# Kernel optimization log

Hardware: AMD Instinct MI355X
Metric: run time of the kernel (lower is better)

The kernel has to match this reference:

```python
import jax, jax.numpy as jnp
import numpy as np

CODEBOOK_SIZE = 8192
EMBED_DIM = 256


def setup_inputs() -> dict:
    key = jax.random.key(0)
    k_rep, k_cb = jax.random.split(key)
    rep = jax.random.normal(k_rep, (32, 2048, EMBED_DIM), dtype=jnp.float32)
    codebook = jax.random.normal(k_cb, (CODEBOOK_SIZE, EMBED_DIM), dtype=jnp.float32)
    return {"rep": rep, "codebook": codebook}


def reference(rep, codebook):
    # rep: [B, M, D], codebook: [K, D]
    B, M, D = rep.shape
    rep_flat = rep.reshape(-1, D)                                # [B*M, D]
    a2 = jnp.sum(rep_flat * rep_flat, axis=1, keepdims=True)     # [B*M, 1]
    b2 = jnp.sum(codebook * codebook, axis=1)[None, :]           # [1, K]
    ab = rep_flat @ codebook.T                                   # [B*M, K]
    dist = a2 + b2 - 2.0 * ab                                    # [B*M, K]
    idx = jnp.argmin(dist, axis=1).reshape(B, M)                 # [B, M] int
    return idx
```

## Files before the change

### kernel.cpp

```cpp
#include <hip/hip_runtime.h>
#include <stdint.h>

#define KCODES 8192
#define DIM 256
#define BM 128
#define BN 128
#define NTHREADS 512
#define NKT (KCODES / BN)
#define NSTEP (NKT * 2)

typedef _Float16 h16;
typedef __attribute__((ext_vector_type(8))) _Float16 f16x8;
typedef __attribute__((ext_vector_type(4))) float f32x4;

__device__ __forceinline__ void split8(const float* __restrict__ x, f16x8& h, f16x8& l) {
    #pragma unroll
    for (int i = 0; i < 8; ++i) {
        float v = x[i];
        _Float16 hv = (_Float16)v;
        h[i] = hv;
        l[i] = (_Float16)(v - (float)hv);
    }
}

__device__ __forceinline__ unsigned int ford(float f) {
    unsigned int b = __float_as_uint(f);
    return (b & 0x80000000u) ? ~b : (b | 0x80000000u);
}

#define WS_C2H   0u
#define WS_LC    32768u
#define WS_CN    65536u
#define WS_CNT   98304u
#define WS_LIST  98560u
#define WS_CAND  360704u
#define WS_THR   622848u
#define WS_KEYS  917504u
#define WS_BPH   2097152u

__global__ __launch_bounds__(256) void c2x_kernel(const float* __restrict__ cb,
                                                  float* __restrict__ c2h,
                                                  float* __restrict__ lc,
                                                  float* __restrict__ cn, int K) {
    int w = (blockIdx.x * blockDim.x + threadIdx.x) >> 6;
    int lane = threadIdx.x & 63;
    if (w >= K) return;
    const float4 v = *(const float4*)(cb + (size_t)w * DIM + lane * 4);
    float s = 0.f, sr = 0.f;
    const float xs[4] = {v.x, v.y, v.z, v.w};
    #pragma unroll
    for (int i = 0; i < 4; ++i) {
        float x = xs[i];
        s += x * x;
        float hf = (float)(_Float16)x;
        float rho = x - hf;
        sr += rho * rho;
    }
    #pragma unroll
    for (int off = 32; off > 0; off >>= 1) { s += __shfl_down(s, off); sr += __shfl_down(sr, off); }
    if (lane == 0) { c2h[w] = 0.5f * s; cn[w] = sqrtf(s); lc[w] = sqrtf(sr); }
}

__global__ __launch_bounds__(256) void pack_h_kernel(const float* __restrict__ cb,
                                                     h16* __restrict__ Bp) {
    const int tid = blockIdx.x * 256 + threadIdx.x;
    const int code = tid >> 5;
    const int grp = tid & 31;
    float x[8];
    *(float4*)&x[0] = *(const float4*)(cb + (size_t)code * DIM + grp * 8);
    *(float4*)&x[4] = *(const float4*)(cb + (size_t)code * DIM + grp * 8 + 4);
    f16x8 hh;
    #pragma unroll
    for (int i = 0; i < 8; ++i) hh[i] = (_Float16)x[i];
    const int kt = code >> 7, col = code & 127;
    const int chunk = grp >> 2, g = grp & 3;
    const int P = kt * 4 + (chunk >> 1);
    const int s = (chunk & 1) * 4 + g;
    const int phys = s ^ (col & 7);
    *(f16x8*)(Bp + (size_t)P * 8192 + col * 64 + phys * 8) = hh;
}

__global__ __launch_bounds__(NTHREADS, 2) void vq_pass1(
    const float* __restrict__ rep, const h16* __restrict__ Bp,
    const float* __restrict__ c2h, const float* __restrict__ lcA,
    const float* __restrict__ cnA, int* __restrict__ cand,
    float* __restrict__ thr) {

    __shared__ __align__(16) h16 dbuf[2][16384];

    const int t = threadIdx.x;
    const int lane = t & 63;
    const int c15 = lane & 15;
    const int g = lane >> 4;
    const int w = t >> 6;
    const int wrow = (w >> 1) * 32;
    const int wcol = (w & 1) * 64;
    const int row0 = blockIdx.x * BM;

    f16x8 ah[2][8];
    float hn[2], rn[2];
    #pragma unroll
    for (int m = 0; m < 2; ++m) {
        const float* ar = rep + (size_t)(row0 + wrow + m * 16 + c15) * DIM + g * 8;
        float hs = 0.f, rs = 0.f;
        #pragma unroll
        for (int ch = 0; ch < 8; ++ch) {
            float x[8];
            *(float4*)&x[0] = *(const float4*)(ar + ch * 32);
            *(float4*)&x[4] = *(const float4*)(ar + ch * 32 + 4);
            #pragma unroll
            for (int i = 0; i < 8; ++i) {
                _Float16 hv = (_Float16)x[i];
                ah[m][ch][i] = hv;
                float hf = (float)hv;
                hs += hf * hf;
                float rho = x[i] - hf;
                rs += rho * rho;
            }
        }
        hs += __shfl_xor(hs, 16); hs += __shfl_xor(hs, 32);
        rs += __shfl_xor(rs, 16); rs += __shfl_xor(rs, 32);
        hn[m] = sqrtf(hs); rn[m] = sqrtf(rs);
    }

    f32x4 acc[2][4];
    float u1v[2][4], u2v[2][4], B2[2][4];
    int u1i[2][4];
    #pragma unroll
    for (int m = 0; m < 2; ++m)
        #pragma unroll
        for (int n = 0; n < 4; ++n) {
            #pragma unroll
            for (int r = 0; r < 4; ++r) acc[m][n][r] = 0.f;
            u1v[m][n] = -3.4e38f; u2v[m][n] = -3.4e38f; u1i[m][n] = 0;
        }

    auto issueStep = [&](int s2, int b) {
        const h16* src = Bp + (size_t)s2 * 16384 + t * 8;
        h16* dst = &dbuf[b][t * 8];
        #pragma unroll
        for (int i = 0; i < 4; ++i)
            __builtin_amdgcn_global_load_lds(
                (const __attribute__((address_space(1))) uint32_t*)(src + i * 4096),
                (__attribute__((address_space(3))) uint32_t*)(dst + i * 4096),
                16, 0, 0);
    };

    asm volatile("s_waitcnt vmcnt(0)" ::: "memory");
    issueStep(0, 0);

    #pragma unroll 1
    for (int kt = 0; kt < NKT; ++kt) {
        const int ktbase = kt * BN;
        #pragma unroll
        for (int q = 0; q < 2; ++q) {
            const int s = kt * 2 + q;
            asm volatile("s_waitcnt vmcnt(0) lgkmcnt(0)" ::: "memory");
            __builtin_amdgcn_s_barrier();
            __builtin_amdgcn_sched_barrier(0);

            if (q == 0) {
                #pragma unroll
                for (int n = 0; n < 4; ++n) {
                    const int col = ktbase + wcol + n * 16 + c15;
                    float cc = c2h[col], lv = lcA[col], cv = cnA[col];
                    #pragma unroll
                    for (int m = 0; m < 2; ++m)
                        B2[m][n] = hn[m] * lv + rn[m] * cv + 0.012f - cc;
                }
            }
            if (s + 1 < NSTEP) issueStep(s + 1, q ^ 1);

            const h16* lb = &dbuf[q][0];
            #pragma unroll
            for (int j = 0; j < 4; ++j) {
                const int ch = q * 4 + j;
                const h16* lp = lb + (j >> 1) * 8192;
                #pragma unroll
                for (int n = 0; n < 4; ++n) {
                    const int base = (wcol + n * 16 + c15) * 64;
                    f16x8 bh = *(const f16x8*)&lp[base + ((((j & 1) * 4 + g) ^ (c15 & 7)) << 3)];
                    #pragma unroll
                    for (int m = 0; m < 2; ++m)
                        acc[m][n] = __builtin_amdgcn_mfma_f32_16x16x32_f16(ah[m][ch], bh, acc[m][n], 0, 0, 0);
                }
            }

            if (q == 1) {
                #pragma unroll
                for (int n = 0; n < 4; ++n) {
                    const int col = ktbase + wcol + n * 16 + c15;
                    #pragma unroll
                    for (int m = 0; m < 2; ++m)
                        #pragma unroll
                        for (int r = 0; r < 4; ++r) {
                            float u = acc[m][n][r] + B2[m][n];
                            if (u > u1v[m][r]) { u2v[m][r] = u1v[m][r]; u1v[m][r] = u; u1i[m][r] = col; }
                            else if (u > u2v[m][r]) u2v[m][r] = u;
                            acc[m][n][r] = 0.f;
                        }
                }
            }
        }
    }

    __syncthreads();
    float* sv1 = (float*)&dbuf[0][0];
    int* si1 = (int*)((char*)&dbuf[0][0] + 1024);
    float* sv2 = (float*)((char*)&dbuf[0][0] + 2048);
    #pragma unroll
    for (int m = 0; m < 2; ++m)
        #pragma unroll
        for (int r = 0; r < 4; ++r) {
            float a1 = u1v[m][r], a2 = u2v[m][r];
            int a1i = u1i[m][r];
            #pragma unroll
            for (int mask = 1; mask <= 8; mask <<= 1) {
                float b1 = __shfl_xor(a1, mask);
                int b1i = __shfl_xor(a1i, mask);
                float b2 = __shfl_xor(a2, mask);
                if (b1 > a1) { a2 = fmaxf(a1, b2); a1 = b1; a1i = b1i; }
                else         { a2 = fmaxf(b1, a2); }
            }
            if (c15 == 0) {
                const int rl = wrow + m * 16 + g * 4 + r;
                sv1[rl * 2 + (w & 1)] = a1;
                si1[rl * 2 + (w & 1)] = a1i;
                sv2[rl * 2 + (w & 1)] = a2;
            }
        }
    __syncthreads();
    if (t < BM) {
        float a1 = sv1[t * 2], a2 = sv2[t * 2];
        int a1i = si1[t * 2];
        float b1 = sv1[t * 2 + 1], b2 = sv2[t * 2 + 1];
        int b1i = si1[t * 2 + 1];
        float u1, u2; int u1idx;
        if (b1 > a1) { u1 = b1; u1idx = b1i; u2 = fmaxf(a1, b2); }
        else         { u1 = a1; u1idx = a1i; u2 = fmaxf(b1, a2); }
        cand[row0 + t] = u1idx;
        thr[row0 + t] = u2;
    }
}

__global__ __launch_bounds__(256) void resolve_kernel(
    const float* __restrict__ rep, const float* __restrict__ cb,
    const float* __restrict__ c2h, const int* __restrict__ cand,
    const float* __restrict__ thr, int* __restrict__ out,
    int* __restrict__ cnt, int* __restrict__ list, int N) {
    const int W = (blockIdx.x * 256 + threadIdx.x) >> 6;
    const int lane = threadIdx.x & 63;
    if (W >= N) return;
    const int ci = cand[W];
    const float4 rv = *(const float4*)(rep + (size_t)W * DIM + lane * 4);
    const float4 cv = *(const float4*)(cb + (size_t)ci * DIM + lane * 4);
    float p = rv.x * cv.x + rv.y * cv.y + rv.z * cv.z + rv.w * cv.w;
    #pragma unroll
    for (int off = 32; off > 0; off >>= 1) p += __shfl_down(p, off);
    if (lane == 0) {
        float sex = p - c2h[ci];
        out[W] = ci;
        if (!(sex > thr[W])) {
            int pos = atomicAdd(cnt, 1);
            list[pos] = W;
        }
    }
}

__global__ __launch_bounds__(256) void rescan_kernel(
    const float* __restrict__ rep, const float* __restrict__ cb,
    const float* __restrict__ c2h, const int* __restrict__ cnt_p,
    const int* __restrict__ list, unsigned long long* __restrict__ keys) {

    const int cnt = *cnt_p;
    const int base = blockIdx.x * 64;
    if (base >= cnt) return;
    const int nrows = min(64, cnt - base);
    const int ktbase = (int)blockIdx.y * BN;

    __shared__ __align__(16) h16 lds[2][BN * 64];
    const int t = threadIdx.x;
    const int lane = t & 63;
    const int w = t >> 6;
    const int c15 = lane & 15;
    const int g = lane >> 4;
    const int wrow = w * 16;

    const int aslot = wrow + c15;
    const int grow = list[base + (aslot < nrows ? aslot : 0)];
    f16x8 ah[8], al[8];
    {
        const float* ar = rep + (size_t)grow * DIM + g * 8;
        #pragma unroll
        for (int ch = 0; ch < 8; ++ch) {
            float x[8];
            *(float4*)&x[0] = *(const float4*)(ar + ch * 32);
            *(float4*)&x[4] = *(const float4*)(ar + ch * 32 + 4);
            split8(x, ah[ch], al[ch]);
        }
    }
    f32x4 acc[8];
    float cc[8];
    #pragma unroll
    for (int n = 0; n < 8; ++n) {
        #pragma unroll
        for (int r = 0; r < 4; ++r) acc[n][r] = 0.f;
        cc[n] = c2h[ktbase + n * 16 + c15];
    }

    const int scol = t >> 1;
    const int dslot = t & 1;
    float breg[16];
    auto loadB = [&](int ch) {
        const float* src = cb + (size_t)(ktbase + scol) * DIM + ch * 32 + dslot * 16;
        #pragma unroll
        for (int i = 0; i < 4; ++i) *(float4*)&breg[i * 4] = *(const float4*)(src + i * 4);
    };
    auto writeB = [&](int buf) {
        #pragma unroll
        for (int half = 0; half < 2; ++half) {
            f16x8 hh, ll;
            split8(&breg[half * 8], hh, ll);
            const int s = dslot * 2 + half;
            *(f16x8*)&lds[buf][scol * 64 + ((s ^ (scol & 7)) << 3)] = hh;
            *(f16x8*)&lds[buf][scol * 64 + (((s + 4) ^ (scol & 7)) << 3)] = ll;
        }
    };

    loadB(0);
    writeB(0);
    loadB(1);
    __syncthreads();

    #pragma unroll
    for (int chunk = 0; chunk < 8; ++chunk) {
        const int buf = chunk & 1;
        if (chunk != 7) writeB(buf ^ 1);
        if (chunk <= 5) loadB(chunk + 2);
        #pragma unroll
        for (int n = 0; n < 8; ++n) {
            const int bb = (n * 16 + c15) * 64;
            f16x8 bh = *(const f16x8*)&lds[buf][bb + ((g ^ (lane & 7)) << 3)];
            f16x8 bl = *(const f16x8*)&lds[buf][bb + (((4 + g) ^ (lane & 7)) << 3)];
            acc[n] = __builtin_amdgcn_mfma_f32_16x16x32_f16(ah[chunk], bh, acc[n], 0, 0, 0);
            acc[n] = __builtin_amdgcn_mfma_f32_16x16x32_f16(ah[chunk], bl, acc[n], 0, 0, 0);
            acc[n] = __builtin_amdgcn_mfma_f32_16x16x32_f16(al[chunk], bh, acc[n], 0, 0, 0);
            acc[n] = __builtin_amdgcn_mfma_f32_16x16x32_f16(al[chunk], bl, acc[n], 0, 0, 0);
        }
        __syncthreads();
    }

    #pragma unroll
    for (int r = 0; r < 4; ++r) {
        float bv = -3.4e38f;
        int bi = 0;
        #pragma unroll
        for (int n = 0; n < 8; ++n) {
            float s2 = acc[n][r] - cc[n];
            const int col = ktbase + n * 16 + c15;
            if (s2 > bv) { bv = s2; bi = col; }
        }
        #pragma unroll
        for (int mask = 1; mask <= 8; mask <<= 1) {
            float ov = __shfl_xor(bv, mask);
            int oi = __shfl_xor(bi, mask);
            if (ov > bv || (ov == bv && oi < bi)) { bv = ov; bi = oi; }
        }
        const int oslot = wrow + g * 4 + r;
        if (c15 == 0 && oslot < nrows) {
            unsigned long long key =
                ((unsigned long long)ford(bv) << 32) | (unsigned int)(~(unsigned int)bi);
            atomicMax(&keys[list[base + oslot]], key);
        }
    }
}

__global__ __launch_bounds__(256) void writeback_kernel(
    const int* __restrict__ cnt_p, const int* __restrict__ list,
    const unsigned long long* __restrict__ keys, int* __restrict__ out) {
    int i = blockIdx.x * 256 + threadIdx.x;
    if (i >= *cnt_p) return;
    int row = list[i];
    out[row] = (int)(~(unsigned int)(keys[row] & 0xFFFFFFFFull));
}

extern "C" void kernel_launch(void* const* d_in, const int* in_sizes, int n_in,
                              void* d_out, int out_size, void* d_ws, size_t ws_size,
                              hipStream_t stream) {
    const float* rep = (const float*)d_in[0];
    const float* cb = (const float*)d_in[1];
    const int N = in_sizes[0] / DIM;
    const int K = in_sizes[1] / DIM;
    char* ws = (char*)d_ws;
    float* c2h = (float*)(ws + WS_C2H);
    float* lc  = (float*)(ws + WS_LC);
    float* cn  = (float*)(ws + WS_CN);
    int* cnt   = (int*)(ws + WS_CNT);
    int* list  = (int*)(ws + WS_LIST);
    int* cand  = (int*)(ws + WS_CAND);
    float* thr = (float*)(ws + WS_THR);
    unsigned long long* keys = (unsigned long long*)(ws + WS_KEYS);
    h16* Bph   = (h16*)(ws + WS_BPH);
    int* out = (int*)d_out;

    c2x_kernel<<<dim3((K * 64 + 255) / 256), dim3(256), 0, stream>>>(cb, c2h, lc, cn, K);
    pack_h_kernel<<<dim3(KCODES * 32 / 256), dim3(256), 0, stream>>>(cb, Bph);
    hipMemsetAsync(cnt, 0, sizeof(int), stream);
    hipMemsetAsync(keys, 0, (size_t)N * sizeof(unsigned long long), stream);
    vq_pass1<<<dim3(N / BM), dim3(NTHREADS), 0, stream>>>(rep, Bph, c2h, lc, cn, cand, thr);
    resolve_kernel<<<dim3(N / 4), dim3(256), 0, stream>>>(rep, cb, c2h, cand, thr, out, cnt, list, N);
    rescan_kernel<<<dim3(N / 64, NKT), dim3(256), 0, stream>>>(rep, cb, c2h, cnt, list, keys);
    writeback_kernel<<<dim3(N / 256), dim3(256), 0, stream>>>(cnt, list, keys, out);
}
```

Before: 534.8 us.

## Shrink pass1 blocks to 64 rows and use a 3-slot LDS ring with prefetch distance two

The main distance kernel now runs 256-thread blocks covering 64 rows instead of 512-thread blocks covering 128 rows. Codebook tiles are streamed in quarter-size steps through a three-slot LDS ring, prefetched two steps ahead, with a partial vmcnt wait in place of a full drain every step. The aim is to keep more loads in flight and fit more blocks per CU, hiding global-to-LDS latency. The cost is twice as many codebook reads overall, since each block reuses every tile across only half as many rows, plus more barriers per tile.

Result: no change. 524.8 us (-1.9%).

```diff
diff --git a/kernel.cpp b/kernel.cpp
--- a/kernel.cpp
+++ b/kernel.cpp
@@ -3,11 +3,9 @@
 
 #define KCODES 8192
 #define DIM 256
-#define BM 128
 #define BN 128
-#define NTHREADS 512
 #define NKT (KCODES / BN)
-#define NSTEP (NKT * 2)
+#define NSTEP (NKT * 4)
 
 typedef _Float16 h16;
 typedef __attribute__((ext_vector_type(8))) _Float16 f16x8;
@@ -80,13 +78,13 @@
     *(f16x8*)(Bp + (size_t)P * 8192 + col * 64 + phys * 8) = hh;
 }
 
-__global__ __launch_bounds__(NTHREADS, 2) void vq_pass1(
+__global__ __launch_bounds__(256, 3) void vq_pass1(
     const float* __restrict__ rep, const h16* __restrict__ Bp,
     const float* __restrict__ c2h, const float* __restrict__ lcA,
     const float* __restrict__ cnA, int* __restrict__ cand,
     float* __restrict__ thr) {
 
-    __shared__ __align__(16) h16 dbuf[2][16384];
+    __shared__ __align__(16) h16 ring[3][8192];
 
     const int t = threadIdx.x;
     const int lane = t & 63;
@@ -95,7 +93,7 @@
     const int w = t >> 6;
     const int wrow = (w >> 1) * 32;
     const int wcol = (w & 1) * 64;
-    const int row0 = blockIdx.x * BM;
+    const int row0 = blockIdx.x * 64;
 
     f16x8 ah[2][8];
     float hn[2], rn[2];
@@ -135,31 +133,34 @@
             u1v[m][n] = -3.4e38f; u2v[m][n] = -3.4e38f; u1i[m][n] = 0;
         }
 
-    auto issueStep = [&](int s2, int b) {
-        const h16* src = Bp + (size_t)s2 * 16384 + t * 8;
-        h16* dst = &dbuf[b][t * 8];
+    auto issueStep = [&](int s2, int slot) {
+        const h16* src = Bp + (size_t)s2 * 8192 + t * 8;
+        h16* dst = &ring[slot][t * 8];
         #pragma unroll
         for (int i = 0; i < 4; ++i)
             __builtin_amdgcn_global_load_lds(
-                (const __attribute__((address_space(1))) uint32_t*)(src + i * 4096),
-                (__attribute__((address_space(3))) uint32_t*)(dst + i * 4096),
+                (const __attribute__((address_space(1))) uint32_t*)(src + i * 2048),
+                (__attribute__((address_space(3))) uint32_t*)(dst + i * 2048),
                 16, 0, 0);
     };
 
     asm volatile("s_waitcnt vmcnt(0)" ::: "memory");
     issueStep(0, 0);
-
+    issueStep(1, 1);
+
+    int bufq = 0;
     #pragma unroll 1
     for (int kt = 0; kt < NKT; ++kt) {
         const int ktbase = kt * BN;
         #pragma unroll
-        for (int q = 0; q < 2; ++q) {
-            const int s = kt * 2 + q;
-            asm volatile("s_waitcnt vmcnt(0) lgkmcnt(0)" ::: "memory");
+        for (int cp = 0; cp < 4; ++cp) {
+            const int s = kt * 4 + cp;
+            if (s == NSTEP - 1) asm volatile("s_waitcnt vmcnt(0) lgkmcnt(0)" ::: "memory");
+            else                asm volatile("s_waitcnt vmcnt(4) lgkmcnt(0)" ::: "memory");
             __builtin_amdgcn_s_barrier();
             __builtin_amdgcn_sched_barrier(0);
 
-            if (q == 0) {
+            if (cp == 0) {
                 #pragma unroll
                 for (int n = 0; n < 4; ++n) {
                     const int col = ktbase + wcol + n * 16 + c15;
@@ -169,24 +170,27 @@
                         B2[m][n] = hn[m] * lv + rn[m] * cv + 0.012f - cc;
                 }
             }
-            if (s + 1 < NSTEP) issueStep(s + 1, q ^ 1);
-
-            const h16* lb = &dbuf[q][0];
+            if (s + 2 < NSTEP) {
+                int slot = bufq + 2;
+                if (slot >= 3) slot -= 3;
+                issueStep(s + 2, slot);
+            }
+
+            const h16* lb = &ring[bufq][0];
             #pragma unroll
-            for (int j = 0; j < 4; ++j) {
-                const int ch = q * 4 + j;
-                const h16* lp = lb + (j >> 1) * 8192;
+            for (int j = 0; j < 2; ++j) {
+                const int ch = cp * 2 + j;
                 #pragma unroll
                 for (int n = 0; n < 4; ++n) {
                     const int base = (wcol + n * 16 + c15) * 64;
-                    f16x8 bh = *(const f16x8*)&lp[base + ((((j & 1) * 4 + g) ^ (c15 & 7)) << 3)];
+                    f16x8 bh = *(const f16x8*)&lb[base + (((j * 4 + g) ^ (c15 & 7)) << 3)];
                     #pragma unroll
                     for (int m = 0; m < 2; ++m)
                         acc[m][n] = __builtin_amdgcn_mfma_f32_16x16x32_f16(ah[m][ch], bh, acc[m][n], 0, 0, 0);
                 }
             }
 
-            if (q == 1) {
+            if (cp == 3) {
                 #pragma unroll
                 for (int n = 0; n < 4; ++n) {
                     const int col = ktbase + wcol + n * 16 + c15;
@@ -201,13 +205,14 @@
                         }
                 }
             }
+            bufq = (bufq + 1 == 3) ? 0 : bufq + 1;
         }
     }
 
     __syncthreads();
-    float* sv1 = (float*)&dbuf[0][0];
-    int* si1 = (int*)((char*)&dbuf[0][0] + 1024);
-    float* sv2 = (float*)((char*)&dbuf[0][0] + 2048);
+    float* sv1 = (float*)&ring[0][0];
+    int* si1 = (int*)((char*)&ring[0][0] + 1024);
+    float* sv2 = (float*)((char*)&ring[0][0] + 2048);
     #pragma unroll
     for (int m = 0; m < 2; ++m)
         #pragma unroll
@@ -230,7 +235,7 @@
             }
         }
     __syncthreads();
-    if (t < BM) {
+    if (t < 64) {
         float a1 = sv1[t * 2], a2 = sv2[t * 2];
         int a1i = si1[t * 2];
         float b1 = sv1[t * 2 + 1], b2 = sv2[t * 2 + 1];
@@ -407,7 +412,7 @@
     pack_h_kernel<<<dim3(KCODES * 32 / 256), dim3(256), 0, stream>>>(cb, Bph);
     hipMemsetAsync(cnt, 0, sizeof(int), stream);
     hipMemsetAsync(keys, 0, (size_t)N * sizeof(unsigned long long), stream);
-    vq_pass1<<<dim3(N / BM), dim3(NTHREADS), 0, stream>>>(rep, Bph, c2h, lc, cn, cand, thr);
+    vq_pass1<<<dim3(N / 64), dim3(256), 0, stream>>>(rep, Bph, c2h, lc, cn, cand, thr);
     resolve_kernel<<<dim3(N / 4), dim3(256), 0, stream>>>(rep, cb, c2h, cand, thr, out, cnt, list, N);
     rescan_kernel<<<dim3(N / 64, NKT), dim3(256), 0, stream>>>(rep, cb, c2h, cnt, list, keys);
     writeback_kernel<<<dim3(N / 256), dim3(256), 0, stream>>>(cnt, list, keys, out);
```
